# Optimization experiments

Measured on AMD Instinct MI355X. Metric: run time of the kernel, lower is better.

## Reference

```python
import jax, jax.numpy as jnp
import numpy as np

N_NODES = 100000
N_EDGES = 1600000
IN_C, HID_C, OUT_C = 128, 64, 32


def setup_inputs() -> dict:
    key = jax.random.key(0)
    k0, k1, k2, k3 = jax.random.split(key, 4)
    x = jax.random.normal(k0, (N_NODES, IN_C), dtype=jnp.float32)
    edge_index = jax.random.randint(k1, (2, N_EDGES), 0, N_NODES, dtype=jnp.int32)
    # Glorot-ish init for GCNConv weights, zero bias (PyG default bias init is zeros)
    W1 = jax.random.normal(k2, (IN_C, HID_C), dtype=jnp.float32) * (1.0 / np.sqrt(IN_C))
    b1 = jnp.zeros((HID_C,), dtype=jnp.float32)
    W2 = jax.random.normal(k3, (HID_C, OUT_C), dtype=jnp.float32) * (1.0 / np.sqrt(HID_C))
    b2 = jnp.zeros((OUT_C,), dtype=jnp.float32)
    return {"x": x, "edge_index": edge_index, "W1": W1, "b1": b1, "W2": W2, "b2": b2}


def reference(x, edge_index, W1, b1, W2, b2):
    n = x.shape[0]
    # GCNConv default: add self-loops, then symmetric normalization D^-1/2 A D^-1/2
    loop = jnp.arange(n, dtype=edge_index.dtype)
    src = jnp.concatenate([edge_index[0], loop])  # message sources (j)
    dst = jnp.concatenate([edge_index[1], loop])  # aggregation targets (i)
    deg = jax.ops.segment_sum(jnp.ones(src.shape, x.dtype), dst, num_segments=n)
    inv_sqrt = jnp.where(deg > 0, jax.lax.rsqrt(deg), 0.0)
    norm = inv_sqrt[src] * inv_sqrt[dst]  # [E+N]

    def gcn_conv(h, W, b):
        h = h @ W  # transform first (smaller feature dim for aggregation)
        msgs = h[src] * norm[:, None]  # gather + scale, [E+N, d]
        agg = jax.ops.segment_sum(msgs, dst, num_segments=n)  # scatter-add
        return agg + b

    h = jax.nn.relu(gcn_conv(x, W1, b1))
    return gcn_conv(h, W2, b2)
```

## Files before the change

### kernel.cpp

```cpp
#include <hip/hip_runtime.h>

#define N_NODES 100000
#define N_EDGES 1600000
#define NCOARSE 391
#define CB_NODES 256
#define CSTRIPE 8
#define CCAP    704
#define CSTRIDE 5632
#define BCHUNKS 256
#define BCHUNK  6250
#define NSTRIPS 6250

typedef short short8 __attribute__((ext_vector_type(8)));
typedef float f32x4 __attribute__((ext_vector_type(4)));
union Frag { uint4 q; short8 s; };

__device__ inline unsigned short f2bf(float f) {
    unsigned u = __float_as_uint(f);
    unsigned r = u + 0x7fffu + ((u >> 16) & 1u);
    return (unsigned short)(r >> 16);
}
__device__ inline unsigned pk2(float lo, float hi) {
    return (unsigned)f2bf(lo) | ((unsigned)f2bf(hi) << 16);
}
__device__ inline float bflo(unsigned u) { return __uint_as_float(u << 16); }
__device__ inline float bfhi(unsigned u) { return __uint_as_float(u & 0xffff0000u); }

__global__ __launch_bounds__(256) void k_prep(const float* __restrict__ W1, const float* __restrict__ W2,
                                              unsigned* __restrict__ W1f, unsigned* __restrict__ W2f,
                                              int* __restrict__ cbcnt) {
    int f = blockIdx.x;
    int t = threadIdx.x;
    if (f >= 20) {
        int i = (f - 20) * 256 + t;
        if (i < NCOARSE * CSTRIPE) cbcnt[i] = 0;
        return;
    }
    int lane = t >> 2, w = t & 3;
    if (f < 16) {
        int ks = f >> 2, ct = f & 3;
        int col = ct * 16 + (lane & 15);
        int k = ks * 32 + (lane >> 4) * 8 + 2 * w;
        W1f[(f * 64 + lane) * 4 + w] = pk2(W1[k * 64 + col], W1[(k + 1) * 64 + col]);
    } else {
        int f2 = f - 16;
        int ks = f2 >> 1, ct = f2 & 1;
        int col = ct * 16 + (lane & 15);
        int k = ks * 32 + (lane >> 4) * 8 + 2 * w;
        W2f[(f2 * 64 + lane) * 4 + w] = pk2(W2[k * 32 + col], W2[(k + 1) * 32 + col]);
    }
}

__global__ __launch_bounds__(512) void k_bin(const int* __restrict__ ei, unsigned* __restrict__ pairs,
                                             int* __restrict__ cbcnt) {
    __shared__ int hist[NCOARSE];
    __shared__ int base[NCOARSE];
    int t = threadIdx.x;
    int chunk = blockIdx.x;
    int s = chunk & (CSTRIPE - 1);
    int e0 = chunk * BCHUNK;
    int e1 = e0 + BCHUNK;
    for (int i = t; i < NCOARSE; i += 512) hist[i] = 0;
    __syncthreads();
#pragma unroll 4
    for (int e = e0 + t; e < e1; e += 512) {
        atomicAdd(&hist[ei[N_EDGES + e] >> 8], 1);
    }
    __syncthreads();
    for (int i = t; i < NCOARSE; i += 512) {
        int h = hist[i];
        if (h > 0) base[i] = atomicAdd(&cbcnt[i * CSTRIPE + s], h);
        hist[i] = 0;
    }
    __syncthreads();
#pragma unroll 2
    for (int e = e0 + t; e < e1; e += 512) {
        int src = ei[e];
        int dst = ei[N_EDGES + e];
        int b = dst >> 8;
        int r = atomicAdd(&hist[b], 1);
        int pos = base[b] + r;
        if (pos < CCAP)
            pairs[(size_t)(b * CSTRIPE + s) * CCAP + pos] = ((unsigned)src << 8) | (unsigned)(dst & 255);
    }
}

__global__ __launch_bounds__(256) void k_csr(const unsigned* __restrict__ pairs, const int* __restrict__ cbcnt,
                                             int* __restrict__ cols, int2* __restrict__ rpc,
                                             float* __restrict__ invs) {
    __shared__ unsigned ep[CSTRIDE];
    __shared__ unsigned srt[CSTRIDE];
    __shared__ int scnt[CSTRIPE];
    __shared__ int sbase[CSTRIPE + 1];
    __shared__ int cnt[CB_NODES];
    __shared__ int cur[CB_NODES];
    __shared__ int wsum[4];
    int t = threadIdx.x;
    int b = blockIdx.x;
    if (t < CSTRIPE) {
        int c = cbcnt[b * CSTRIPE + t];
        scnt[t] = (c < CCAP) ? c : CCAP;
    }
    cnt[t] = 0;
    __syncthreads();
    if (t == 0) {
        int acc = 0;
#pragma unroll
        for (int s = 0; s < CSTRIPE; ++s) { sbase[s] = acc; acc += scnt[s]; }
        sbase[CSTRIPE] = acc;
    }
    __syncthreads();
    int n = sbase[CSTRIPE];
#pragma unroll
    for (int s = 0; s < CSTRIPE; ++s) {
        int cs = scnt[s];
        const unsigned* sp = pairs + (size_t)(b * CSTRIPE + s) * CCAP;
        int base = sbase[s];
        for (int i = t; i < cs; i += 256) ep[base + i] = sp[i];
    }
    __syncthreads();
    for (int i = t; i < n; i += 256) atomicAdd(&cnt[ep[i] & 255u], 1);
    __syncthreads();
    {
        int c = cnt[t];
        int v = c;
#pragma unroll
        for (int off = 1; off < 64; off <<= 1) {
            int u = __shfl_up(v, off, 64);
            if ((t & 63) >= off) v += u;
        }
        if ((t & 63) == 63) wsum[t >> 6] = v;
        __syncthreads();
        int woff = 0;
        for (int w = 0; w < (t >> 6); ++w) woff += wsum[w];
        int excl = woff + v - c;
        cur[t] = excl;
        int node = b * CB_NODES + t;
        if (node < N_NODES) {
            rpc[node] = make_int2(b * CSTRIDE + excl, c);
            invs[node] = rsqrtf((float)(c + 1));
        }
    }
    __syncthreads();
    for (int i = t; i < n; i += 256) {
        unsigned p = ep[i];
        int f = p & 255u;
        int pos = atomicAdd(&cur[f], 1);
        srt[pos] = p >> 8;
    }
    __syncthreads();
    int* outp = cols + (size_t)b * CSTRIDE;
    for (int i = t; i < n; i += 256) outp[i] = (int)srt[i];
}

__global__ __launch_bounds__(256) void k_gemm1(const float* __restrict__ X, const uint4* __restrict__ W1f,
                                               const float* __restrict__ invs, unsigned short* __restrict__ out) {
    __shared__ unsigned short lt[4][16][72];
    int t = threadIdx.x;
    int w = t >> 6, l = t & 63;
    int strip = blockIdx.x * 4 + w;
    if (strip >= NSTRIPS) return;
    const float* xrow = X + (size_t)(strip * 16 + (l & 15)) * 128;
    f32x4 acc[4];
#pragma unroll
    for (int ct = 0; ct < 4; ++ct) acc[ct] = (f32x4){0.f, 0.f, 0.f, 0.f};
#pragma unroll
    for (int ks = 0; ks < 4; ++ks) {
        int kk = ks * 32 + (l >> 4) * 8;
        float4 xa = *(const float4*)(xrow + kk);
        float4 xb = *(const float4*)(xrow + kk + 4);
        Frag fa;
        fa.q = make_uint4(pk2(xa.x, xa.y), pk2(xa.z, xa.w), pk2(xb.x, xb.y), pk2(xb.z, xb.w));
#pragma unroll
        for (int ct = 0; ct < 4; ++ct) {
            Frag fb; fb.q = W1f[(ks * 4 + ct) * 64 + l];
            acc[ct] = __builtin_amdgcn_mfma_f32_16x16x32_bf16(fa.s, fb.s, acc[ct], 0, 0, 0);
        }
    }
    int rbase = strip * 16 + (l >> 4) * 4;
    float iv0 = invs[rbase], iv1 = invs[rbase + 1], iv2 = invs[rbase + 2], iv3 = invs[rbase + 3];
#pragma unroll
    for (int ct = 0; ct < 4; ++ct) {
        int cc = ct * 16 + (l & 15);
        int rr = (l >> 4) * 4;
        lt[w][rr + 0][cc] = f2bf(acc[ct][0] * iv0);
        lt[w][rr + 1][cc] = f2bf(acc[ct][1] * iv1);
        lt[w][rr + 2][cc] = f2bf(acc[ct][2] * iv2);
        lt[w][rr + 3][cc] = f2bf(acc[ct][3] * iv3);
    }
    uint4* og = (uint4*)(out + (size_t)strip * 16 * 64);
#pragma unroll
    for (int it = 0; it < 2; ++it) {
        int idx = it * 64 + l;
        int row = idx >> 3, seg = idx & 7;
        og[idx] = *(const uint4*)&lt[w][row][seg * 8];
    }
}

__global__ __launch_bounds__(256) void k_gemm2(const unsigned short* __restrict__ Xb, const uint4* __restrict__ W2f,
                                               const float* __restrict__ invs, unsigned short* __restrict__ out) {
    __shared__ unsigned short lt[4][16][40];
    int t = threadIdx.x;
    int w = t >> 6, l = t & 63;
    int strip = blockIdx.x * 4 + w;
    if (strip >= NSTRIPS) return;
    const unsigned short* xrow = Xb + (size_t)(strip * 16 + (l & 15)) * 64;
    f32x4 acc[2];
#pragma unroll
    for (int ct = 0; ct < 2; ++ct) acc[ct] = (f32x4){0.f, 0.f, 0.f, 0.f};
#pragma unroll
    for (int ks = 0; ks < 2; ++ks) {
        int kk = ks * 32 + (l >> 4) * 8;
        Frag fa;
        fa.q = *(const uint4*)(xrow + kk);
#pragma unroll
        for (int ct = 0; ct < 2; ++ct) {
            Frag fb; fb.q = W2f[(ks * 2 + ct) * 64 + l];
            acc[ct] = __builtin_amdgcn_mfma_f32_16x16x32_bf16(fa.s, fb.s, acc[ct], 0, 0, 0);
        }
    }
    int rbase = strip * 16 + (l >> 4) * 4;
    float iv0 = invs[rbase], iv1 = invs[rbase + 1], iv2 = invs[rbase + 2], iv3 = invs[rbase + 3];
#pragma unroll
    for (int ct = 0; ct < 2; ++ct) {
        int cc = ct * 16 + (l & 15);
        int rr = (l >> 4) * 4;
        lt[w][rr + 0][cc] = f2bf(acc[ct][0] * iv0);
        lt[w][rr + 1][cc] = f2bf(acc[ct][1] * iv1);
        lt[w][rr + 2][cc] = f2bf(acc[ct][2] * iv2);
        lt[w][rr + 3][cc] = f2bf(acc[ct][3] * iv3);
    }
    uint4* og = (uint4*)(out + (size_t)strip * 16 * 32);
    {
        int row = l >> 2, seg = l & 3;
        og[l] = *(const uint4*)&lt[w][row][seg * 8];
    }
}

__global__ __launch_bounds__(256) void k_spmm1(const unsigned short* __restrict__ hs, const int2* __restrict__ rpc,
                                               const int* __restrict__ col, const float* __restrict__ invs,
                                               const float* __restrict__ b, unsigned short* __restrict__ out) {
    int t = threadIdx.x;
    int l = t & 7;
    int node = blockIdx.x * 32 + (t >> 3);
    int2 rc = rpc[node];
    int ps = rc.x, pe = rc.x + rc.y;
    const uint4* hv = (const uint4*)hs;
    float a0 = 0.f, a1 = 0.f, a2 = 0.f, a3 = 0.f, a4 = 0.f, a5 = 0.f, a6 = 0.f, a7 = 0.f;
    int p = ps;
    for (; p + 4 <= pe; p += 4) {
        int j0 = col[p], j1 = col[p + 1], j2 = col[p + 2], j3 = col[p + 3];
        uint4 u0 = hv[(size_t)j0 * 8 + l];
        uint4 u1 = hv[(size_t)j1 * 8 + l];
        uint4 u2 = hv[(size_t)j2 * 8 + l];
        uint4 u3 = hv[(size_t)j3 * 8 + l];
        a0 += bflo(u0.x); a1 += bfhi(u0.x); a2 += bflo(u0.y); a3 += bfhi(u0.y);
        a4 += bflo(u0.z); a5 += bfhi(u0.z); a6 += bflo(u0.w); a7 += bfhi(u0.w);
        a0 += bflo(u1.x); a1 += bfhi(u1.x); a2 += bflo(u1.y); a3 += bfhi(u1.y);
        a4 += bflo(u1.z); a5 += bfhi(u1.z); a6 += bflo(u1.w); a7 += bfhi(u1.w);
        a0 += bflo(u2.x); a1 += bfhi(u2.x); a2 += bflo(u2.y); a3 += bfhi(u2.y);
        a4 += bflo(u2.z); a5 += bfhi(u2.z); a6 += bflo(u2.w); a7 += bfhi(u2.w);
        a0 += bflo(u3.x); a1 += bfhi(u3.x); a2 += bflo(u3.y); a3 += bfhi(u3.y);
        a4 += bflo(u3.z); a5 += bfhi(u3.z); a6 += bflo(u3.w); a7 += bfhi(u3.w);
    }
    for (; p < pe; ++p) {
        uint4 u = hv[(size_t)col[p] * 8 + l];
        a0 += bflo(u.x); a1 += bfhi(u.x); a2 += bflo(u.y); a3 += bfhi(u.y);
        a4 += bflo(u.z); a5 += bfhi(u.z); a6 += bflo(u.w); a7 += bfhi(u.w);
    }
    uint4 us = hv[(size_t)node * 8 + l];
    a0 += bflo(us.x); a1 += bfhi(us.x); a2 += bflo(us.y); a3 += bfhi(us.y);
    a4 += bflo(us.z); a5 += bfhi(us.z); a6 += bflo(us.w); a7 += bfhi(us.w);
    float iv = invs[node];
    float4 bb0 = *(const float4*)&b[l * 8];
    float4 bb1 = *(const float4*)&b[l * 8 + 4];
    float o0 = fmaxf(a0 * iv + bb0.x, 0.f), o1 = fmaxf(a1 * iv + bb0.y, 0.f);
    float o2 = fmaxf(a2 * iv + bb0.z, 0.f), o3 = fmaxf(a3 * iv + bb0.w, 0.f);
    float o4 = fmaxf(a4 * iv + bb1.x, 0.f), o5 = fmaxf(a5 * iv + bb1.y, 0.f);
    float o6 = fmaxf(a6 * iv + bb1.z, 0.f), o7 = fmaxf(a7 * iv + bb1.w, 0.f);
    uint4 ow;
    ow.x = pk2(o0, o1); ow.y = pk2(o2, o3); ow.z = pk2(o4, o5); ow.w = pk2(o6, o7);
    ((uint4*)out)[(size_t)node * 8 + l] = ow;
}

__global__ __launch_bounds__(256) void k_spmm2(const unsigned short* __restrict__ hs, const int2* __restrict__ rpc,
                                               const int* __restrict__ col, const float* __restrict__ invs,
                                               const float* __restrict__ b, float* __restrict__ out) {
    int t = threadIdx.x;
    int l = t & 3;
    int node = blockIdx.x * 64 + (t >> 2);
    if (node >= N_NODES) return;
    int2 rc = rpc[node];
    int ps = rc.x, pe = rc.x + rc.y;
    const uint4* hv = (const uint4*)hs;
    float a0 = 0.f, a1 = 0.f, a2 = 0.f, a3 = 0.f, a4 = 0.f, a5 = 0.f, a6 = 0.f, a7 = 0.f;
    int p = ps;
    for (; p + 4 <= pe; p += 4) {
        int j0 = col[p], j1 = col[p + 1], j2 = col[p + 2], j3 = col[p + 3];
        uint4 u0 = hv[(size_t)j0 * 4 + l];
        uint4 u1 = hv[(size_t)j1 * 4 + l];
        uint4 u2 = hv[(size_t)j2 * 4 + l];
        uint4 u3 = hv[(size_t)j3 * 4 + l];
        a0 += bflo(u0.x); a1 += bfhi(u0.x); a2 += bflo(u0.y); a3 += bfhi(u0.y);
        a4 += bflo(u0.z); a5 += bfhi(u0.z); a6 += bflo(u0.w); a7 += bfhi(u0.w);
        a0 += bflo(u1.x); a1 += bfhi(u1.x); a2 += bflo(u1.y); a3 += bfhi(u1.y);
        a4 += bflo(u1.z); a5 += bfhi(u1.z); a6 += bflo(u1.w); a7 += bfhi(u1.w);
        a0 += bflo(u2.x); a1 += bfhi(u2.x); a2 += bflo(u2.y); a3 += bfhi(u2.y);
        a4 += bflo(u2.z); a5 += bfhi(u2.z); a6 += bflo(u2.w); a7 += bfhi(u2.w);
        a0 += bflo(u3.x); a1 += bfhi(u3.x); a2 += bflo(u3.y); a3 += bfhi(u3.y);
        a4 += bflo(u3.z); a5 += bfhi(u3.z); a6 += bflo(u3.w); a7 += bfhi(u3.w);
    }
    for (; p < pe; ++p) {
        uint4 u = hv[(size_t)col[p] * 4 + l];
        a0 += bflo(u.x); a1 += bfhi(u.x); a2 += bflo(u.y); a3 += bfhi(u.y);
        a4 += bflo(u.z); a5 += bfhi(u.z); a6 += bflo(u.w); a7 += bfhi(u.w);
    }
    uint4 us = hv[(size_t)node * 4 + l];
    a0 += bflo(us.x); a1 += bfhi(us.x); a2 += bflo(us.y); a3 += bfhi(us.y);
    a4 += bflo(us.z); a5 += bfhi(us.z); a6 += bflo(us.w); a7 += bfhi(us.w);
    float iv = invs[node];
    float4 bb0 = *(const float4*)&b[l * 8];
    float4 bb1 = *(const float4*)&b[l * 8 + 4];
    float4 oA = make_float4(a0 * iv + bb0.x, a1 * iv + bb0.y, a2 * iv + bb0.z, a3 * iv + bb0.w);
    float4 oB = make_float4(a4 * iv + bb1.x, a5 * iv + bb1.y, a6 * iv + bb1.z, a7 * iv + bb1.w);
    *(float4*)&out[(size_t)node * 32 + l * 8] = oA;
    *(float4*)&out[(size_t)node * 32 + l * 8 + 4] = oB;
}

extern "C" void kernel_launch(void* const* d_in, const int* in_sizes, int n_in,
                              void* d_out, int out_size, void* d_ws, size_t ws_size,
                              hipStream_t stream) {
    const float* x  = (const float*)d_in[0];
    const int*   ei = (const int*)d_in[1];
    const float* W1 = (const float*)d_in[2];
    const float* b1 = (const float*)d_in[3];
    const float* W2 = (const float*)d_in[4];
    const float* b2 = (const float*)d_in[5];
    float* out = (float*)d_out;

    char* ws = (char*)d_ws;
    size_t off = 0;
    auto alloc = [&](size_t bytes) -> void* {
        void* p = ws + off;
        off = (off + bytes + 255) & ~(size_t)255;
        return p;
    };
    int*            cbcnt = (int*)alloc((size_t)NCOARSE * CSTRIPE * 4);
    float*          invs  = (float*)alloc((size_t)N_NODES * 4);
    unsigned*       pairs = (unsigned*)alloc((size_t)NCOARSE * CSTRIPE * CCAP * 4);
    int*            cols  = (int*)alloc((size_t)NCOARSE * CSTRIDE * 4);
    int2*           rpc   = (int2*)alloc((size_t)N_NODES * 8);
    unsigned short* hs1   = (unsigned short*)alloc((size_t)N_NODES * 64 * 2);
    unsigned short* h2bf  = (unsigned short*)alloc((size_t)N_NODES * 64 * 2);
    unsigned*       W1f   = (unsigned*)alloc(16 * 64 * 16);
    unsigned*       W2f   = (unsigned*)alloc(4 * 64 * 16);
    unsigned short* hs2   = hs1;

    k_prep<<<20 + (NCOARSE * CSTRIPE + 255) / 256, 256, 0, stream>>>(W1, W2, W1f, W2f, cbcnt);
    k_bin<<<BCHUNKS, 512, 0, stream>>>(ei, pairs, cbcnt);
    k_csr<<<NCOARSE, 256, 0, stream>>>(pairs, cbcnt, cols, rpc, invs);
    k_gemm1<<<(NSTRIPS + 3) / 4, 256, 0, stream>>>(x, (const uint4*)W1f, invs, hs1);
    k_spmm1<<<N_NODES / 32, 256, 0, stream>>>(hs1, rpc, cols, invs, b1, h2bf);
    k_gemm2<<<(NSTRIPS + 3) / 4, 256, 0, stream>>>(h2bf, (const uint4*)W2f, invs, hs2);
    k_spmm2<<<(N_NODES + 63) / 64, 256, 0, stream>>>(hs2, rpc, cols, invs, b2, out);
}
```

Measured before the change: 116.3 us.

## Fuse layer-1 aggregation with second GEMM and vectorize CSR copies

The layer-1 SpMM is merged with the second-layer transform. Each block aggregates 32 nodes into shared memory as bf16, then runs MFMA against W2, which is staged in LDS, and writes the scaled 32-wide output directly. This removes a kernel launch and the global round-trip of the 64-wide hidden activations. The CSR build kernel also gets uint4-vectorized copies for the pair loads and the column writes. In exchange the fused kernel adds a block-wide barrier and scattered 2-byte output stores.

```diff
diff --git a/kernel.cpp b/kernel.cpp
--- a/kernel.cpp
+++ b/kernel.cpp
@@ -115,8 +115,15 @@
     for (int s = 0; s < CSTRIPE; ++s) {
         int cs = scnt[s];
         const unsigned* sp = pairs + (size_t)(b * CSTRIPE + s) * CCAP;
+        const uint4* sp4 = (const uint4*)sp;
         int base = sbase[s];
-        for (int i = t; i < cs; i += 256) ep[base + i] = sp[i];
+        int cs4 = cs >> 2;
+        for (int i = t; i < cs4; i += 256) {
+            uint4 v = sp4[i];
+            int o = base + i * 4;
+            ep[o] = v.x; ep[o + 1] = v.y; ep[o + 2] = v.z; ep[o + 3] = v.w;
+        }
+        for (int i = cs4 * 4 + t; i < cs; i += 256) ep[base + i] = sp[i];
     }
     __syncthreads();
     for (int i = t; i < n; i += 256) atomicAdd(&cnt[ep[i] & 255u], 1);
@@ -150,7 +157,13 @@
     }
     __syncthreads();
     int* outp = cols + (size_t)b * CSTRIDE;
-    for (int i = t; i < n; i += 256) outp[i] = (int)srt[i];
+    uint4* outp4 = (uint4*)outp;
+    int n4 = n >> 2;
+    for (int i = t; i < n4; i += 256) {
+        int o = i * 4;
+        outp4[i] = make_uint4(srt[o], srt[o + 1], srt[o + 2], srt[o + 3]);
+    }
+    for (int i = n4 * 4 + t; i < n; i += 256) outp[i] = (int)srt[i];
 }
 
 __global__ __launch_bounds__(256) void k_gemm1(const float* __restrict__ X, const uint4* __restrict__ W1f,
@@ -197,52 +210,18 @@
     }
 }
 
-__global__ __launch_bounds__(256) void k_gemm2(const unsigned short* __restrict__ Xb, const uint4* __restrict__ W2f,
-                                               const float* __restrict__ invs, unsigned short* __restrict__ out) {
-    __shared__ unsigned short lt[4][16][40];
-    int t = threadIdx.x;
-    int w = t >> 6, l = t & 63;
-    int strip = blockIdx.x * 4 + w;
-    if (strip >= NSTRIPS) return;
-    const unsigned short* xrow = Xb + (size_t)(strip * 16 + (l & 15)) * 64;
-    f32x4 acc[2];
-#pragma unroll
-    for (int ct = 0; ct < 2; ++ct) acc[ct] = (f32x4){0.f, 0.f, 0.f, 0.f};
-#pragma unroll
-    for (int ks = 0; ks < 2; ++ks) {
-        int kk = ks * 32 + (l >> 4) * 8;
-        Frag fa;
-        fa.q = *(const uint4*)(xrow + kk);
-#pragma unroll
-        for (int ct = 0; ct < 2; ++ct) {
-            Frag fb; fb.q = W2f[(ks * 2 + ct) * 64 + l];
-            acc[ct] = __builtin_amdgcn_mfma_f32_16x16x32_bf16(fa.s, fb.s, acc[ct], 0, 0, 0);
-        }
-    }
-    int rbase = strip * 16 + (l >> 4) * 4;
-    float iv0 = invs[rbase], iv1 = invs[rbase + 1], iv2 = invs[rbase + 2], iv3 = invs[rbase + 3];
-#pragma unroll
-    for (int ct = 0; ct < 2; ++ct) {
-        int cc = ct * 16 + (l & 15);
-        int rr = (l >> 4) * 4;
-        lt[w][rr + 0][cc] = f2bf(acc[ct][0] * iv0);
-        lt[w][rr + 1][cc] = f2bf(acc[ct][1] * iv1);
-        lt[w][rr + 2][cc] = f2bf(acc[ct][2] * iv2);
-        lt[w][rr + 3][cc] = f2bf(acc[ct][3] * iv3);
-    }
-    uint4* og = (uint4*)(out + (size_t)strip * 16 * 32);
-    {
-        int row = l >> 2, seg = l & 3;
-        og[l] = *(const uint4*)&lt[w][row][seg * 8];
-    }
-}
-
-__global__ __launch_bounds__(256) void k_spmm1(const unsigned short* __restrict__ hs, const int2* __restrict__ rpc,
-                                               const int* __restrict__ col, const float* __restrict__ invs,
-                                               const float* __restrict__ b, unsigned short* __restrict__ out) {
-    int t = threadIdx.x;
+__global__ __launch_bounds__(256) void k_l1(const unsigned short* __restrict__ hs, const int2* __restrict__ rpc,
+                                            const int* __restrict__ col, const float* __restrict__ invs,
+                                            const float* __restrict__ b1, const uint4* __restrict__ W2f,
+                                            unsigned short* __restrict__ out) {
+    __shared__ unsigned short hsh[32][72];
+    __shared__ float ivsh[32];
+    __shared__ uint4 w2sh[256];
+    int t = threadIdx.x;
+    w2sh[t] = W2f[t];
     int l = t & 7;
-    int node = blockIdx.x * 32 + (t >> 3);
+    int g = t >> 3;
+    int node = blockIdx.x * 32 + g;
     int2 rc = rpc[node];
     int ps = rc.x, pe = rc.x + rc.y;
     const uint4* hv = (const uint4*)hs;
@@ -272,15 +251,33 @@
     a0 += bflo(us.x); a1 += bfhi(us.x); a2 += bflo(us.y); a3 += bfhi(us.y);
     a4 += bflo(us.z); a5 += bfhi(us.z); a6 += bflo(us.w); a7 += bfhi(us.w);
     float iv = invs[node];
-    float4 bb0 = *(const float4*)&b[l * 8];
-    float4 bb1 = *(const float4*)&b[l * 8 + 4];
-    float o0 = fmaxf(a0 * iv + bb0.x, 0.f), o1 = fmaxf(a1 * iv + bb0.y, 0.f);
-    float o2 = fmaxf(a2 * iv + bb0.z, 0.f), o3 = fmaxf(a3 * iv + bb0.w, 0.f);
-    float o4 = fmaxf(a4 * iv + bb1.x, 0.f), o5 = fmaxf(a5 * iv + bb1.y, 0.f);
-    float o6 = fmaxf(a6 * iv + bb1.z, 0.f), o7 = fmaxf(a7 * iv + bb1.w, 0.f);
-    uint4 ow;
-    ow.x = pk2(o0, o1); ow.y = pk2(o2, o3); ow.z = pk2(o4, o5); ow.w = pk2(o6, o7);
-    ((uint4*)out)[(size_t)node * 8 + l] = ow;
+    float4 bb0 = *(const float4*)&b1[l * 8];
+    float4 bb1 = *(const float4*)&b1[l * 8 + 4];
+    float h0 = fmaxf(a0 * iv + bb0.x, 0.f), h1 = fmaxf(a1 * iv + bb0.y, 0.f);
+    float h2 = fmaxf(a2 * iv + bb0.z, 0.f), h3 = fmaxf(a3 * iv + bb0.w, 0.f);
+    float h4 = fmaxf(a4 * iv + bb1.x, 0.f), h5 = fmaxf(a5 * iv + bb1.y, 0.f);
+    float h6 = fmaxf(a6 * iv + bb1.z, 0.f), h7 = fmaxf(a7 * iv + bb1.w, 0.f);
+    uint4 hw;
+    hw.x = pk2(h0, h1); hw.y = pk2(h2, h3); hw.z = pk2(h4, h5); hw.w = pk2(h6, h7);
+    *(uint4*)&hsh[g][l * 8] = hw;
+    if (l == 0) ivsh[g] = iv;
+    __syncthreads();
+    int wv = t >> 6, lane = t & 63;
+    int rt = wv & 1, ct = wv >> 1;
+    f32x4 acc = (f32x4){0.f, 0.f, 0.f, 0.f};
+#pragma unroll
+    for (int ks = 0; ks < 2; ++ks) {
+        Frag fa; fa.q = *(const uint4*)&hsh[rt * 16 + (lane & 15)][ks * 32 + (lane >> 4) * 8];
+        Frag fb; fb.q = w2sh[(ks * 2 + ct) * 64 + lane];
+        acc = __builtin_amdgcn_mfma_f32_16x16x32_bf16(fa.s, fb.s, acc, 0, 0, 0);
+    }
+    int rl = rt * 16 + (lane >> 4) * 4;
+    size_t nodeo = (size_t)(blockIdx.x * 32 + rl);
+    int cc = ct * 16 + (lane & 15);
+    out[(nodeo + 0) * 32 + cc] = f2bf(acc[0] * ivsh[rl + 0]);
+    out[(nodeo + 1) * 32 + cc] = f2bf(acc[1] * ivsh[rl + 1]);
+    out[(nodeo + 2) * 32 + cc] = f2bf(acc[2] * ivsh[rl + 2]);
+    out[(nodeo + 3) * 32 + cc] = f2bf(acc[3] * ivsh[rl + 3]);
 }
 
 __global__ __launch_bounds__(256) void k_spmm2(const unsigned short* __restrict__ hs, const int2* __restrict__ rpc,
@@ -351,16 +348,14 @@
     int*            cols  = (int*)alloc((size_t)NCOARSE * CSTRIDE * 4);
     int2*           rpc   = (int2*)alloc((size_t)N_NODES * 8);
     unsigned short* hs1   = (unsigned short*)alloc((size_t)N_NODES * 64 * 2);
-    unsigned short* h2bf  = (unsigned short*)alloc((size_t)N_NODES * 64 * 2);
+    unsigned short* hs2   = (unsigned short*)alloc((size_t)N_NODES * 32 * 2);
     unsigned*       W1f   = (unsigned*)alloc(16 * 64 * 16);
     unsigned*       W2f   = (unsigned*)alloc(4 * 64 * 16);
-    unsigned short* hs2   = hs1;
 
     k_prep<<<20 + (NCOARSE * CSTRIPE + 255) / 256, 256, 0, stream>>>(W1, W2, W1f, W2f, cbcnt);
     k_bin<<<BCHUNKS, 512, 0, stream>>>(ei, pairs, cbcnt);
     k_csr<<<NCOARSE, 256, 0, stream>>>(pairs, cbcnt, cols, rpc, invs);
     k_gemm1<<<(NSTRIPS + 3) / 4, 256, 0, stream>>>(x, (const uint4*)W1f, invs, hs1);
-    k_spmm1<<<N_NODES / 32, 256, 0, stream>>>(hs1, rpc, cols, invs, b1, h2bf);
-    k_gemm2<<<(NSTRIPS + 3) / 4, 256, 0, stream>>>(h2bf, (const uint4*)W2f, invs, hs2);
+    k_l1<<<N_NODES / 32, 256, 0, stream>>>(hs1, rpc, cols, invs, b1, (const uint4*)W2f, hs2);
     k_spmm2<<<(N_NODES + 63) / 64, 256, 0, stream>>>(hs2, rpc, cols, invs, b2, out);
 }
```

Measured after the change: 108.0 us. -7.1%, faster.
